# Optimization experiments

Measured on AMD Instinct MI355X. Metric: run time of the kernel, lower is better.

The kernel has to match this reference:

```python
import jax, jax.numpy as jnp
import numpy as np

N_NODES = 100000
N_EDGES = 1600000
N_GRAPHS = 512


def setup_inputs() -> dict:
    key = jax.random.key(0)
    k = jax.random.split(key, 6)
    x = jax.random.normal(k[0], (N_NODES, 768), dtype=jnp.float32)
    edge_index = jax.random.randint(k[1], (2, N_EDGES), 0, N_NODES, dtype=jnp.int32)
    batch = jnp.sort(jax.random.randint(k[2], (N_NODES,), 0, N_GRAPHS, dtype=jnp.int32))
    W1 = jax.random.normal(k[3], (768, 256), dtype=jnp.float32) * 0.02
    b1 = jnp.zeros((256,), dtype=jnp.float32)
    W2 = jax.random.normal(k[4], (256, 2), dtype=jnp.float32) * 0.02
    b2 = jnp.zeros((2,), dtype=jnp.float32)
    return {"x": x, "edge_index": edge_index, "batch": batch,
            "W1": W1, "b1": b1, "W2": W2, "b2": b2}


def gcn_conv(x, src, dst, W, b, n_nodes):
    # PyG GCNConv: h = x @ W; add self-loops; symmetric normalization D^-1/2 A D^-1/2
    h = x @ W  # [N, out]
    ones = jnp.ones((src.shape[0],), dtype=x.dtype)
    # degree including self-loop
    deg = jax.ops.segment_sum(ones, dst, num_segments=n_nodes) + 1.0  # [N]
    dinv = jax.lax.rsqrt(deg)
    norm_e = dinv[src] * dinv[dst]  # [E]
    msg = h[src] * norm_e[:, None]  # gather + scale, [E, out]
    agg = jax.ops.segment_sum(msg, dst, num_segments=n_nodes)  # scatter-add
    # self-loop contribution: norm = dinv[i]*dinv[i] = 1/deg[i]
    agg = agg + h * (1.0 / deg)[:, None]
    return agg + b


def reference(x, edge_index, batch, W1, b1, W2, b2):
    n_nodes = x.shape[0]
    src, dst = edge_index[0], edge_index[1]
    h = gcn_conv(x, src, dst, W1, b1, n_nodes)
    h = jax.nn.relu(h)
    # dropout p=0.5 is identity in eval mode (self.training=False)
    h = gcn_conv(h, src, dst, W2, b2, n_nodes)
    # global_mean_pool over batch assignment
    sums = jax.ops.segment_sum(h, batch, num_segments=N_GRAPHS)  # [G, out]
    counts = jax.ops.segment_sum(jnp.ones((n_nodes,), h.dtype), batch, num_segments=N_GRAPHS)
    return sums / jnp.maximum(counts, 1.0)[:, None]
```

## Files before the change

### kernel.cpp

```cpp
#include <hip/hip_runtime.h>

typedef unsigned short u16;
typedef unsigned int   u32;
typedef __bf16 bf16x8 __attribute__((ext_vector_type(8)));
typedef float  f32x4  __attribute__((ext_vector_type(4)));
typedef u32    u32x4  __attribute__((ext_vector_type(4)));
typedef u16    u16x8  __attribute__((ext_vector_type(8)));

#define NF1 768
#define NF2 256

__device__ __forceinline__ u16 f2bf(float f) {
  u32 u = __builtin_bit_cast(u32, f);
  u += 0x7fffu + ((u >> 16) & 1u);
  return (u16)(u >> 16);
}
__device__ __forceinline__ float bf2f(u16 h) {
  return __builtin_bit_cast(float, ((u32)h) << 16);
}

__device__ __forceinline__ void gll16(const void* g, void* l) {
  __builtin_amdgcn_global_load_lds(
      (const __attribute__((address_space(1))) unsigned int*)g,
      (__attribute__((address_space(3))) unsigned int*)l, 16, 0, 0);
}

__global__ void k_zero(u32* __restrict__ p, int n) {
  int i = blockIdx.x * 256 + threadIdx.x;
  if (i < n) p[i] = 0u;
}

__global__ void k_w1t(const float* __restrict__ W1, u16* __restrict__ W1T) {
  int idx = blockIdx.x * 256 + threadIdx.x;
  if (idx < NF1 * NF2) {
    int k = idx >> 8, j = idx & 255;
    W1T[(size_t)j * NF1 + k] = f2bf(W1[idx]);
  }
}

__global__ __launch_bounds__(512, 1) void k_gemm(const float* __restrict__ X,
                                                 const u16* __restrict__ W1T,
                                                 u16* __restrict__ H1, int M) {
  __shared__ float lsA[256 * 64];
  __shared__ u16   lsB[256 * 64];
  const int t    = threadIdx.x;
  const int m0   = blockIdx.x * 256;
  const int lane = t & 63;
  const int wid  = t >> 6;
  const int wr   = wid >> 1;
  const int wc   = wid & 1;

  const float* srcA[8];
  #pragma unroll
  for (int i = 0; i < 8; ++i) {
    int row_l = wid * 32 + i * 4 + (lane >> 4);
    int perm  = ((row_l & 7) << 1) | ((row_l >> 3) & 1);
    int gr    = m0 + row_l;
    if (gr > M - 1) gr = M - 1;
    srcA[i] = X + (size_t)gr * NF1 + (((lane & 15) ^ perm) * 4);
  }
  const u16* srcB[4];
  #pragma unroll
  for (int j = 0; j < 4; ++j) {
    int col_l = wid * 32 + j * 8 + (lane >> 3);
    srcB[j] = W1T + (size_t)col_l * NF1 + (((lane & 7) ^ (lane >> 3)) * 8);
  }

  f32x4 acc[4][8];
  #pragma unroll
  for (int m = 0; m < 4; ++m)
    #pragma unroll
    for (int n = 0; n < 8; ++n) { f32x4 z = {0.f, 0.f, 0.f, 0.f}; acc[m][n] = z; }

  const int lm     = lane & 15;
  const int l4     = lane >> 4;
  const int perm_r = ((lane & 7) << 1) | ((lane >> 3) & 1);
  const int lp     = lane & 7;

  const int NT = NF1 / 64;
  for (int kt = 0; kt < NT; ++kt) {
    #pragma unroll
    for (int i = 0; i < 8; ++i)
      gll16(srcA[i] + kt * 64, &lsA[(wid * 32 + i * 4) * 64]);
    #pragma unroll
    for (int j = 0; j < 4; ++j)
      gll16(srcB[j] + kt * 64, &lsB[(wid * 32 + j * 8) * 64]);
    __syncthreads();

    #pragma unroll
    for (int ks = 0; ks < 2; ++ks) {
      bf16x8 af[4], bfr[8];
      const int c = ks * 4 + l4;
      #pragma unroll
      for (int m = 0; m < 4; ++m) {
        int row = wr * 64 + m * 16 + lm;
        int ulo = (2 * c) ^ perm_r;
        const char* base = (const char*)lsA + row * 256;
        float4 L = *(const float4*)(base + ulo * 16);
        float4 H = *(const float4*)(base + (ulo ^ 1) * 16);
        u32 w0, w1, w2, w3;
        asm("v_cvt_pk_bf16_f32 %0, %1, %2" : "=v"(w0) : "v"(L.x), "v"(L.y));
        asm("v_cvt_pk_bf16_f32 %0, %1, %2" : "=v"(w1) : "v"(L.z), "v"(L.w));
        asm("v_cvt_pk_bf16_f32 %0, %1, %2" : "=v"(w2) : "v"(H.x), "v"(H.y));
        asm("v_cvt_pk_bf16_f32 %0, %1, %2" : "=v"(w3) : "v"(H.z), "v"(H.w));
        u32x4 uw = {w0, w1, w2, w3};
        af[m] = __builtin_bit_cast(bf16x8, uw);
      }
      #pragma unroll
      for (int n = 0; n < 8; ++n) {
        int col = wc * 128 + n * 16 + lm;
        int ph  = c ^ lp;
        bfr[n] = *(const bf16x8*)((const char*)lsB + col * 128 + ph * 16);
      }
      #pragma unroll
      for (int m = 0; m < 4; ++m)
        #pragma unroll
        for (int n = 0; n < 8; ++n)
          acc[m][n] = __builtin_amdgcn_mfma_f32_16x16x32_bf16(af[m], bfr[n], acc[m][n], 0, 0, 0);
    }
    __syncthreads();
  }

  #pragma unroll
  for (int m = 0; m < 4; ++m) {
    int rowb = m0 + wr * 64 + m * 16 + (lane >> 4) * 4;
    #pragma unroll
    for (int n = 0; n < 8; ++n) {
      int col = wc * 128 + n * 16 + (lane & 15);
      #pragma unroll
      for (int j = 0; j < 4; ++j) {
        int row = rowb + j;
        if (row < M) H1[(size_t)row * NF2 + col] = f2bf(acc[m][n][j]);
      }
    }
  }
}

__global__ void k_deg(const int* __restrict__ EI, int E, u32* __restrict__ deg) {
  int e = blockIdx.x * 256 + threadIdx.x;
  if (e < E) atomicAdd(&deg[EI[E + e]], 1u);
}

__global__ __launch_bounds__(1024) void k_scan1(const u32* __restrict__ deg,
                                                u32* __restrict__ rowptr,
                                                u32* __restrict__ bsum, int Nn) {
  __shared__ u32 sm[1024];
  int t = threadIdx.x;
  int i = blockIdx.x * 1024 + t;
  u32 v = (i < Nn) ? deg[i] : 0u;
  sm[t] = v;
  __syncthreads();
  #pragma unroll
  for (int off = 1; off < 1024; off <<= 1) {
    u32 x = (t >= off) ? sm[t - off] : 0u;
    __syncthreads();
    sm[t] += x;
    __syncthreads();
  }
  u32 incl = sm[t];
  if (i < Nn) rowptr[i] = incl - v;
  if (t == 1023) bsum[blockIdx.x] = incl;
}

__global__ void k_scan2(const u32* __restrict__ bsum, u32* __restrict__ boff, int nc) {
  __shared__ u32 sm[128];
  int t = threadIdx.x;
  u32 v = (t < nc) ? bsum[t] : 0u;
  sm[t] = v;
  __syncthreads();
  #pragma unroll
  for (int off = 1; off < 128; off <<= 1) {
    u32 x = (t >= off) ? sm[t - off] : 0u;
    __syncthreads();
    sm[t] += x;
    __syncthreads();
  }
  if (t < nc) boff[t] = sm[t] - v;
}

__global__ void k_scan3(u32* __restrict__ rowptr, const u32* __restrict__ boff,
                        u32* __restrict__ cursor, const u32* __restrict__ deg,
                        float* __restrict__ dinv, int Nn, int E) {
  int i = blockIdx.x * 256 + threadIdx.x;
  if (i < Nn) {
    u32 rp = rowptr[i] + boff[i >> 10];
    rowptr[i] = rp;
    cursor[i] = rp;
    dinv[i] = rsqrtf((float)deg[i] + 1.0f);
  }
  if (i == 0) rowptr[Nn] = (u32)E;
}

__global__ void k_fill(const int* __restrict__ EI, int E, int* __restrict__ cursor,
                       int* __restrict__ csr) {
  int e = blockIdx.x * 256 + threadIdx.x;
  if (e < E) {
    int s = EI[e], d = EI[E + e];
    int pos = atomicAdd(&cursor[d], 1);
    csr[pos] = s;
  }
}

__global__ __launch_bounds__(256) void k_agg1(const u16* __restrict__ H1,
                                              const int* __restrict__ csr,
                                              const u32* __restrict__ rowptr,
                                              const float* __restrict__ dinv,
                                              const float* __restrict__ B1,
                                              const float* __restrict__ W2,
                                              float* __restrict__ H2, int Nn) {
  int node = (blockIdx.x << 2) + (threadIdx.x >> 6);
  if (node >= Nn) return;
  const int lane = threadIdx.x & 63;
  const int hl   = lane >> 5;
  const int fo   = (lane & 31) * 8;
  const int rp0 = (int)rowptr[node], rp1 = (int)rowptr[node + 1];
  const float dvi = dinv[node];

  float c0 = 0.f, c1 = 0.f, c2 = 0.f, c3 = 0.f,
        c4 = 0.f, c5 = 0.f, c6 = 0.f, c7 = 0.f;

  for (int e = rp0 + 2 * hl; e < rp1; e += 8) {
    const int eA = e, eB = e + 1, eC = e + 4, eD = e + 5;
    const bool hB = eB < rp1, hC = eC < rp1, hD = eD < rp1;
    const int sA = csr[eA];
    const int sB = hB ? csr[eB] : sA;
    const int sC = hC ? csr[eC] : sA;
    const int sD = hD ? csr[eD] : sA;
    const u16x8 rA = *(const u16x8*)(H1 + (size_t)sA * NF2 + fo);
    const u16x8 rB = *(const u16x8*)(H1 + (size_t)sB * NF2 + fo);
    const u16x8 rC = *(const u16x8*)(H1 + (size_t)sC * NF2 + fo);
    const u16x8 rD = *(const u16x8*)(H1 + (size_t)sD * NF2 + fo);
    const float nA = dinv[sA] * dvi;
    const float nB = hB ? dinv[sB] * dvi : 0.f;
    const float nC = hC ? dinv[sC] * dvi : 0.f;
    const float nD = hD ? dinv[sD] * dvi : 0.f;
    c0 += nA * bf2f(rA[0]) + nB * bf2f(rB[0]) + nC * bf2f(rC[0]) + nD * bf2f(rD[0]);
    c1 += nA * bf2f(rA[1]) + nB * bf2f(rB[1]) + nC * bf2f(rC[1]) + nD * bf2f(rD[1]);
    c2 += nA * bf2f(rA[2]) + nB * bf2f(rB[2]) + nC * bf2f(rC[2]) + nD * bf2f(rD[2]);
    c3 += nA * bf2f(rA[3]) + nB * bf2f(rB[3]) + nC * bf2f(rC[3]) + nD * bf2f(rD[3]);
    c4 += nA * bf2f(rA[4]) + nB * bf2f(rB[4]) + nC * bf2f(rC[4]) + nD * bf2f(rD[4]);
    c5 += nA * bf2f(rA[5]) + nB * bf2f(rB[5]) + nC * bf2f(rC[5]) + nD * bf2f(rD[5]);
    c6 += nA * bf2f(rA[6]) + nB * bf2f(rB[6]) + nC * bf2f(rC[6]) + nD * bf2f(rD[6]);
    c7 += nA * bf2f(rA[7]) + nB * bf2f(rB[7]) + nC * bf2f(rC[7]) + nD * bf2f(rD[7]);
  }

  c0 += __shfl_xor(c0, 32);
  c1 += __shfl_xor(c1, 32);
  c2 += __shfl_xor(c2, 32);
  c3 += __shfl_xor(c3, 32);
  c4 += __shfl_xor(c4, 32);
  c5 += __shfl_xor(c5, 32);
  c6 += __shfl_xor(c6, 32);
  c7 += __shfl_xor(c7, 32);

  {
    const float ns = dvi * dvi;
    const u16x8 rs = *(const u16x8*)(H1 + (size_t)node * NF2 + fo);
    c0 += ns * bf2f(rs[0]); c1 += ns * bf2f(rs[1]);
    c2 += ns * bf2f(rs[2]); c3 += ns * bf2f(rs[3]);
    c4 += ns * bf2f(rs[4]); c5 += ns * bf2f(rs[5]);
    c6 += ns * bf2f(rs[6]); c7 += ns * bf2f(rs[7]);
  }

  const float4 bA = *(const float4*)(B1 + fo);
  const float4 bB = *(const float4*)(B1 + fo + 4);
  const float r0 = fmaxf(c0 + bA.x, 0.f), r1 = fmaxf(c1 + bA.y, 0.f);
  const float r2 = fmaxf(c2 + bA.z, 0.f), r3 = fmaxf(c3 + bA.w, 0.f);
  const float r4 = fmaxf(c4 + bB.x, 0.f), r5 = fmaxf(c5 + bB.y, 0.f);
  const float r6 = fmaxf(c6 + bB.z, 0.f), r7 = fmaxf(c7 + bB.w, 0.f);

  const float4* wp = (const float4*)(W2 + 2 * fo);
  const float4 w0 = wp[0], w1 = wp[1], w2 = wp[2], w3 = wp[3];
  float p0 = r0 * w0.x + r1 * w0.z + r2 * w1.x + r3 * w1.z
           + r4 * w2.x + r5 * w2.z + r6 * w3.x + r7 * w3.z;
  float p1 = r0 * w0.y + r1 * w0.w + r2 * w1.y + r3 * w1.w
           + r4 * w2.y + r5 * w2.w + r6 * w3.y + r7 * w3.w;
  #pragma unroll
  for (int o = 16; o; o >>= 1) {
    p0 += __shfl_xor(p0, o);
    p1 += __shfl_xor(p1, o);
  }
  if (lane == 0) {
    H2[2 * (size_t)node]     = p0;
    H2[2 * (size_t)node + 1] = p1;
  }
}

__global__ __launch_bounds__(256) void k_l2e(const int* __restrict__ EI, int E,
                                             const float* __restrict__ dinv,
                                             const float* __restrict__ H2,
                                             const int* __restrict__ batch,
                                             float* __restrict__ accg) {
  __shared__ float sb[1024];
  for (int i = threadIdx.x; i < 1024; i += 256) sb[i] = 0.f;
  __syncthreads();
  for (int e = blockIdx.x * 256 + threadIdx.x; e < E; e += gridDim.x * 256) {
    int s = EI[e], d = EI[E + e];
    float nrm = dinv[s] * dinv[d];
    float2 hv = *(const float2*)(H2 + 2 * (size_t)s);
    int g = batch[d];
    atomicAdd(&sb[2 * g],     nrm * hv.x);
    atomicAdd(&sb[2 * g + 1], nrm * hv.y);
  }
  __syncthreads();
  for (int i = threadIdx.x; i < 1024; i += 256)
    if (sb[i] != 0.f) atomicAdd(&accg[i], sb[i]);
}

__global__ __launch_bounds__(256) void k_l2n(int Nn, const float* __restrict__ dinv,
                                             const float* __restrict__ H2,
                                             const int* __restrict__ batch,
                                             float* __restrict__ accg,
                                             u32* __restrict__ gcnt) {
  __shared__ float sb[1024];
  __shared__ u32 sc[512];
  for (int i = threadIdx.x; i < 1024; i += 256) sb[i] = 0.f;
  for (int i = threadIdx.x; i < 512; i += 256) sc[i] = 0u;
  __syncthreads();
  for (int i = blockIdx.x * 256 + threadIdx.x; i < Nn; i += gridDim.x * 256) {
    int g = batch[i];
    float dv = dinv[i];
    float ns = dv * dv;
    float2 hv = *(const float2*)(H2 + 2 * (size_t)i);
    atomicAdd(&sb[2 * g],     ns * hv.x);
    atomicAdd(&sb[2 * g + 1], ns * hv.y);
    atomicAdd(&sc[g], 1u);
  }
  __syncthreads();
  for (int i = threadIdx.x; i < 1024; i += 256)
    if (sb[i] != 0.f) atomicAdd(&accg[i], sb[i]);
  for (int i = threadIdx.x; i < 512; i += 256)
    if (sc[i]) atomicAdd(&gcnt[i], sc[i]);
}

__global__ void k_final(const float* __restrict__ accg, const u32* __restrict__ gcnt,
                        const float* __restrict__ B2, float* __restrict__ out) {
  int i = blockIdx.x * 256 + threadIdx.x;
  if (i < 1024) {
    int g = i >> 1, c = i & 1;
    float cnt = (float)gcnt[g];
    float s = accg[i] + cnt * B2[c];
    out[i] = s / fmaxf(cnt, 1.0f);
  }
}

extern "C" void kernel_launch(void* const* d_in, const int* in_sizes, int n_in,
                              void* d_out, int out_size, void* d_ws, size_t ws_size,
                              hipStream_t stream) {
  const float* X     = (const float*)d_in[0];
  const int*   EI    = (const int*)d_in[1];
  const int*   BATCH = (const int*)d_in[2];
  const float* W1    = (const float*)d_in[3];
  const float* B1    = (const float*)d_in[4];
  const float* W2    = (const float*)d_in[5];
  const float* B2    = (const float*)d_in[6];
  const int Nn = in_sizes[0] / NF1;
  const int E  = in_sizes[1] / 2;
  float* OUT = (float*)d_out;
  (void)n_in; (void)out_size; (void)ws_size;

  char* w = (char*)d_ws;
  size_t off = 0;
  auto alloc = [&](size_t bytes) -> void* {
    void* p = w + off;
    off = (off + bytes + 511) & ~(size_t)511;
    return p;
  };
  u32*   deg    = (u32*)alloc((size_t)Nn * 4);
  u32*   rowptr = (u32*)alloc(((size_t)Nn + 1) * 4);
  u32*   cursor = (u32*)alloc((size_t)Nn * 4);
  u32*   bsum   = (u32*)alloc(512);
  u32*   boff   = (u32*)alloc(512);
  float* dinv   = (float*)alloc((size_t)Nn * 4);
  int*   csr    = (int*)alloc((size_t)E * 4);
  u16*   H1     = (u16*)alloc((size_t)Nn * NF2 * 2);
  float* H2     = (float*)alloc((size_t)Nn * 2 * 4);
  float* accg   = (float*)alloc(1536 * 4);
  u32*   gcnt   = (u32*)(accg + 1024);
  u16*   W1T    = (u16*)alloc((size_t)NF1 * NF2 * 2);

  const int NC = (Nn + 1023) >> 10;

  hipLaunchKernelGGL(k_zero, dim3((Nn + 255) / 256), dim3(256), 0, stream, deg, Nn);
  hipLaunchKernelGGL(k_zero, dim3(6), dim3(256), 0, stream, (u32*)accg, 1536);
  hipLaunchKernelGGL(k_w1t, dim3((NF1 * NF2 + 255) / 256), dim3(256), 0, stream, W1, W1T);
  hipLaunchKernelGGL(k_gemm, dim3((Nn + 255) / 256), dim3(512), 0, stream, X, W1T, H1, Nn);
  hipLaunchKernelGGL(k_deg, dim3((E + 255) / 256), dim3(256), 0, stream, EI, E, deg);
  hipLaunchKernelGGL(k_scan1, dim3(NC), dim3(1024), 0, stream, deg, rowptr, bsum, Nn);
  hipLaunchKernelGGL(k_scan2, dim3(1), dim3(128), 0, stream, bsum, boff, NC);
  hipLaunchKernelGGL(k_scan3, dim3((Nn + 255) / 256), dim3(256), 0, stream,
                     rowptr, boff, cursor, deg, dinv, Nn, E);
  hipLaunchKernelGGL(k_fill, dim3((E + 255) / 256), dim3(256), 0, stream,
                     EI, E, (int*)cursor, csr);
  hipLaunchKernelGGL(k_agg1, dim3((Nn + 3) / 4), dim3(256), 0, stream,
                     H1, csr, rowptr, dinv, B1, W2, H2, Nn);
  hipLaunchKernelGGL(k_l2e, dim3(512), dim3(256), 0, stream, EI, E, dinv, H2, BATCH, accg);
  hipLaunchKernelGGL(k_l2n, dim3(256), dim3(256), 0, stream, Nn, dinv, H2, BATCH, accg, gcnt);
  hipLaunchKernelGGL(k_final, dim3(4), dim3(256), 0, stream, accg, gcnt, B2, OUT);
}
```

Baseline: 474.8 us.

## Prescale GEMM rows by dinv, widen gather unroll, fuse layer-2 pooling kernels

The GEMM epilogue now multiplies each row by dinv[row], so the aggregation kernel no longer loads dinv per neighbour. It just sums pre-scaled rows and applies the destination dinv once at the end. Out-of-range edges are redirected to a zero padding row, and the loop is unrolled to 8 edges per iteration for more memory parallelism. The two layer-2 pooling kernels are merged into one that reads dinv and graph id packed together in PB, and G2 is stored pre-scaled by dinv. Rounding to bf16 after scaling changes numerics slightly, and the GEMM now has to wait for the degree scan.

```diff
diff --git a/kernel.cpp b/kernel.cpp
--- a/kernel.cpp
+++ b/kernel.cpp
@@ -40,7 +40,8 @@
 
 __global__ __launch_bounds__(512, 1) void k_gemm(const float* __restrict__ X,
                                                  const u16* __restrict__ W1T,
-                                                 u16* __restrict__ H1, int M) {
+                                                 const float* __restrict__ dinv,
+                                                 u16* __restrict__ H1s, int M) {
   __shared__ float lsA[256 * 64];
   __shared__ u16   lsB[256 * 64];
   const int t    = threadIdx.x;
@@ -125,12 +126,15 @@
   for (int m = 0; m < 4; ++m) {
     int rowb = m0 + wr * 64 + m * 16 + (lane >> 4) * 4;
     #pragma unroll
-    for (int n = 0; n < 8; ++n) {
-      int col = wc * 128 + n * 16 + (lane & 15);
-      #pragma unroll
-      for (int j = 0; j < 4; ++j) {
-        int row = rowb + j;
-        if (row < M) H1[(size_t)row * NF2 + col] = f2bf(acc[m][n][j]);
+    for (int j = 0; j < 4; ++j) {
+      int row = rowb + j;
+      if (row < M) {
+        float dv = dinv[row];
+        #pragma unroll
+        for (int n = 0; n < 8; ++n) {
+          int col = wc * 128 + n * 16 + (lane & 15);
+          H1s[(size_t)row * NF2 + col] = f2bf(dv * acc[m][n][j]);
+        }
       }
     }
   }
@@ -180,13 +184,17 @@
 
 __global__ void k_scan3(u32* __restrict__ rowptr, const u32* __restrict__ boff,
                         u32* __restrict__ cursor, const u32* __restrict__ deg,
-                        float* __restrict__ dinv, int Nn, int E) {
+                        float* __restrict__ dinv, const int* __restrict__ batch,
+                        float* __restrict__ PB, int Nn, int E) {
   int i = blockIdx.x * 256 + threadIdx.x;
   if (i < Nn) {
     u32 rp = rowptr[i] + boff[i >> 10];
     rowptr[i] = rp;
     cursor[i] = rp;
-    dinv[i] = rsqrtf((float)deg[i] + 1.0f);
+    float dv = rsqrtf((float)deg[i] + 1.0f);
+    dinv[i] = dv;
+    PB[2 * i]     = dv;
+    PB[2 * i + 1] = __builtin_bit_cast(float, batch[i]);
   }
   if (i == 0) rowptr[Nn] = (u32)E;
 }
@@ -201,13 +209,13 @@
   }
 }
 
-__global__ __launch_bounds__(256) void k_agg1(const u16* __restrict__ H1,
+__global__ __launch_bounds__(256) void k_agg1(const u16* __restrict__ H1s,
                                               const int* __restrict__ csr,
                                               const u32* __restrict__ rowptr,
                                               const float* __restrict__ dinv,
                                               const float* __restrict__ B1,
                                               const float* __restrict__ W2,
-                                              float* __restrict__ H2, int Nn) {
+                                              float* __restrict__ G2, int Nn) {
   int node = (blockIdx.x << 2) + (threadIdx.x >> 6);
   if (node >= Nn) return;
   const int lane = threadIdx.x & 63;
@@ -219,29 +227,41 @@
   float c0 = 0.f, c1 = 0.f, c2 = 0.f, c3 = 0.f,
         c4 = 0.f, c5 = 0.f, c6 = 0.f, c7 = 0.f;
 
-  for (int e = rp0 + 2 * hl; e < rp1; e += 8) {
-    const int eA = e, eB = e + 1, eC = e + 4, eD = e + 5;
-    const bool hB = eB < rp1, hC = eC < rp1, hD = eD < rp1;
+  for (int e = rp0 + 2 * hl; e < rp1; e += 16) {
+    const int eA = e,      eB = e + 1,  eC = e + 4,  eD = e + 5;
+    const int eE = e + 8,  eF = e + 9,  eG = e + 12, eH = e + 13;
     const int sA = csr[eA];
-    const int sB = hB ? csr[eB] : sA;
-    const int sC = hC ? csr[eC] : sA;
-    const int sD = hD ? csr[eD] : sA;
-    const u16x8 rA = *(const u16x8*)(H1 + (size_t)sA * NF2 + fo);
-    const u16x8 rB = *(const u16x8*)(H1 + (size_t)sB * NF2 + fo);
-    const u16x8 rC = *(const u16x8*)(H1 + (size_t)sC * NF2 + fo);
-    const u16x8 rD = *(const u16x8*)(H1 + (size_t)sD * NF2 + fo);
-    const float nA = dinv[sA] * dvi;
-    const float nB = hB ? dinv[sB] * dvi : 0.f;
-    const float nC = hC ? dinv[sC] * dvi : 0.f;
-    const float nD = hD ? dinv[sD] * dvi : 0.f;
-    c0 += nA * bf2f(rA[0]) + nB * bf2f(rB[0]) + nC * bf2f(rC[0]) + nD * bf2f(rD[0]);
-    c1 += nA * bf2f(rA[1]) + nB * bf2f(rB[1]) + nC * bf2f(rC[1]) + nD * bf2f(rD[1]);
-    c2 += nA * bf2f(rA[2]) + nB * bf2f(rB[2]) + nC * bf2f(rC[2]) + nD * bf2f(rD[2]);
-    c3 += nA * bf2f(rA[3]) + nB * bf2f(rB[3]) + nC * bf2f(rC[3]) + nD * bf2f(rD[3]);
-    c4 += nA * bf2f(rA[4]) + nB * bf2f(rB[4]) + nC * bf2f(rC[4]) + nD * bf2f(rD[4]);
-    c5 += nA * bf2f(rA[5]) + nB * bf2f(rB[5]) + nC * bf2f(rC[5]) + nD * bf2f(rD[5]);
-    c6 += nA * bf2f(rA[6]) + nB * bf2f(rB[6]) + nC * bf2f(rC[6]) + nD * bf2f(rD[6]);
-    c7 += nA * bf2f(rA[7]) + nB * bf2f(rB[7]) + nC * bf2f(rC[7]) + nD * bf2f(rD[7]);
+    const int sB = (eB < rp1) ? csr[eB] : Nn;
+    const int sC = (eC < rp1) ? csr[eC] : Nn;
+    const int sD = (eD < rp1) ? csr[eD] : Nn;
+    const int sE = (eE < rp1) ? csr[eE] : Nn;
+    const int sF = (eF < rp1) ? csr[eF] : Nn;
+    const int sG = (eG < rp1) ? csr[eG] : Nn;
+    const int sH = (eH < rp1) ? csr[eH] : Nn;
+    const u16x8 rA = *(const u16x8*)(H1s + (size_t)sA * NF2 + fo);
+    const u16x8 rB = *(const u16x8*)(H1s + (size_t)sB * NF2 + fo);
+    const u16x8 rC = *(const u16x8*)(H1s + (size_t)sC * NF2 + fo);
+    const u16x8 rD = *(const u16x8*)(H1s + (size_t)sD * NF2 + fo);
+    const u16x8 rE = *(const u16x8*)(H1s + (size_t)sE * NF2 + fo);
+    const u16x8 rF = *(const u16x8*)(H1s + (size_t)sF * NF2 + fo);
+    const u16x8 rG = *(const u16x8*)(H1s + (size_t)sG * NF2 + fo);
+    const u16x8 rH = *(const u16x8*)(H1s + (size_t)sH * NF2 + fo);
+    c0 += bf2f(rA[0]) + bf2f(rB[0]) + bf2f(rC[0]) + bf2f(rD[0])
+        + bf2f(rE[0]) + bf2f(rF[0]) + bf2f(rG[0]) + bf2f(rH[0]);
+    c1 += bf2f(rA[1]) + bf2f(rB[1]) + bf2f(rC[1]) + bf2f(rD[1])
+        + bf2f(rE[1]) + bf2f(rF[1]) + bf2f(rG[1]) + bf2f(rH[1]);
+    c2 += bf2f(rA[2]) + bf2f(rB[2]) + bf2f(rC[2]) + bf2f(rD[2])
+        + bf2f(rE[2]) + bf2f(rF[2]) + bf2f(rG[2]) + bf2f(rH[2]);
+    c3 += bf2f(rA[3]) + bf2f(rB[3]) + bf2f(rC[3]) + bf2f(rD[3])
+        + bf2f(rE[3]) + bf2f(rF[3]) + bf2f(rG[3]) + bf2f(rH[3]);
+    c4 += bf2f(rA[4]) + bf2f(rB[4]) + bf2f(rC[4]) + bf2f(rD[4])
+        + bf2f(rE[4]) + bf2f(rF[4]) + bf2f(rG[4]) + bf2f(rH[4]);
+    c5 += bf2f(rA[5]) + bf2f(rB[5]) + bf2f(rC[5]) + bf2f(rD[5])
+        + bf2f(rE[5]) + bf2f(rF[5]) + bf2f(rG[5]) + bf2f(rH[5]);
+    c6 += bf2f(rA[6]) + bf2f(rB[6]) + bf2f(rC[6]) + bf2f(rD[6])
+        + bf2f(rE[6]) + bf2f(rF[6]) + bf2f(rG[6]) + bf2f(rH[6]);
+    c7 += bf2f(rA[7]) + bf2f(rB[7]) + bf2f(rC[7]) + bf2f(rD[7])
+        + bf2f(rE[7]) + bf2f(rF[7]) + bf2f(rG[7]) + bf2f(rH[7]);
   }
 
   c0 += __shfl_xor(c0, 32);
@@ -254,20 +274,19 @@
   c7 += __shfl_xor(c7, 32);
 
   {
-    const float ns = dvi * dvi;
-    const u16x8 rs = *(const u16x8*)(H1 + (size_t)node * NF2 + fo);
-    c0 += ns * bf2f(rs[0]); c1 += ns * bf2f(rs[1]);
-    c2 += ns * bf2f(rs[2]); c3 += ns * bf2f(rs[3]);
-    c4 += ns * bf2f(rs[4]); c5 += ns * bf2f(rs[5]);
-    c6 += ns * bf2f(rs[6]); c7 += ns * bf2f(rs[7]);
+    const u16x8 rs = *(const u16x8*)(H1s + (size_t)node * NF2 + fo);
+    c0 += bf2f(rs[0]); c1 += bf2f(rs[1]);
+    c2 += bf2f(rs[2]); c3 += bf2f(rs[3]);
+    c4 += bf2f(rs[4]); c5 += bf2f(rs[5]);
+    c6 += bf2f(rs[6]); c7 += bf2f(rs[7]);
   }
 
   const float4 bA = *(const float4*)(B1 + fo);
   const float4 bB = *(const float4*)(B1 + fo + 4);
-  const float r0 = fmaxf(c0 + bA.x, 0.f), r1 = fmaxf(c1 + bA.y, 0.f);
-  const float r2 = fmaxf(c2 + bA.z, 0.f), r3 = fmaxf(c3 + bA.w, 0.f);
-  const float r4 = fmaxf(c4 + bB.x, 0.f), r5 = fmaxf(c5 + bB.y, 0.f);
-  const float r6 = fmaxf(c6 + bB.z, 0.f), r7 = fmaxf(c7 + bB.w, 0.f);
+  const float r0 = fmaxf(dvi * c0 + bA.x, 0.f), r1 = fmaxf(dvi * c1 + bA.y, 0.f);
+  const float r2 = fmaxf(dvi * c2 + bA.z, 0.f), r3 = fmaxf(dvi * c3 + bA.w, 0.f);
+  const float r4 = fmaxf(dvi * c4 + bB.x, 0.f), r5 = fmaxf(dvi * c5 + bB.y, 0.f);
+  const float r6 = fmaxf(dvi * c6 + bB.z, 0.f), r7 = fmaxf(dvi * c7 + bB.w, 0.f);
 
   const float4* wp = (const float4*)(W2 + 2 * fo);
   const float4 w0 = wp[0], w1 = wp[1], w2 = wp[2], w3 = wp[3];
@@ -281,49 +300,36 @@
     p1 += __shfl_xor(p1, o);
   }
   if (lane == 0) {
-    H2[2 * (size_t)node]     = p0;
-    H2[2 * (size_t)node + 1] = p1;
-  }
-}
-
-__global__ __launch_bounds__(256) void k_l2e(const int* __restrict__ EI, int E,
-                                             const float* __restrict__ dinv,
-                                             const float* __restrict__ H2,
-                                             const int* __restrict__ batch,
-                                             float* __restrict__ accg) {
-  __shared__ float sb[1024];
-  for (int i = threadIdx.x; i < 1024; i += 256) sb[i] = 0.f;
-  __syncthreads();
-  for (int e = blockIdx.x * 256 + threadIdx.x; e < E; e += gridDim.x * 256) {
-    int s = EI[e], d = EI[E + e];
-    float nrm = dinv[s] * dinv[d];
-    float2 hv = *(const float2*)(H2 + 2 * (size_t)s);
-    int g = batch[d];
-    atomicAdd(&sb[2 * g],     nrm * hv.x);
-    atomicAdd(&sb[2 * g + 1], nrm * hv.y);
-  }
-  __syncthreads();
-  for (int i = threadIdx.x; i < 1024; i += 256)
-    if (sb[i] != 0.f) atomicAdd(&accg[i], sb[i]);
-}
-
-__global__ __launch_bounds__(256) void k_l2n(int Nn, const float* __restrict__ dinv,
-                                             const float* __restrict__ H2,
-                                             const int* __restrict__ batch,
-                                             float* __restrict__ accg,
-                                             u32* __restrict__ gcnt) {
+    G2[2 * (size_t)node]     = dvi * p0;
+    G2[2 * (size_t)node + 1] = dvi * p1;
+  }
+}
+
+__global__ __launch_bounds__(256) void k_l2(const int* __restrict__ EI, int E,
+                                            const float* __restrict__ PB,
+                                            const float* __restrict__ G2,
+                                            int Nn,
+                                            float* __restrict__ accg,
+                                            u32* __restrict__ gcnt) {
   __shared__ float sb[1024];
   __shared__ u32 sc[512];
   for (int i = threadIdx.x; i < 1024; i += 256) sb[i] = 0.f;
   for (int i = threadIdx.x; i < 512; i += 256) sc[i] = 0u;
   __syncthreads();
+  for (int e = blockIdx.x * 256 + threadIdx.x; e < E; e += gridDim.x * 256) {
+    int s = EI[e], d = EI[E + e];
+    float2 pb = *(const float2*)(PB + 2 * (size_t)d);
+    float2 hv = *(const float2*)(G2 + 2 * (size_t)s);
+    int g = __builtin_bit_cast(int, pb.y);
+    atomicAdd(&sb[2 * g],     pb.x * hv.x);
+    atomicAdd(&sb[2 * g + 1], pb.x * hv.y);
+  }
   for (int i = blockIdx.x * 256 + threadIdx.x; i < Nn; i += gridDim.x * 256) {
-    int g = batch[i];
-    float dv = dinv[i];
-    float ns = dv * dv;
-    float2 hv = *(const float2*)(H2 + 2 * (size_t)i);
-    atomicAdd(&sb[2 * g],     ns * hv.x);
-    atomicAdd(&sb[2 * g + 1], ns * hv.y);
+    float2 pb = *(const float2*)(PB + 2 * (size_t)i);
+    float2 hv = *(const float2*)(G2 + 2 * (size_t)i);
+    int g = __builtin_bit_cast(int, pb.y);
+    atomicAdd(&sb[2 * g],     pb.x * hv.x);
+    atomicAdd(&sb[2 * g + 1], pb.x * hv.y);
     atomicAdd(&sc[g], 1u);
   }
   __syncthreads();
@@ -372,9 +378,10 @@
   u32*   bsum   = (u32*)alloc(512);
   u32*   boff   = (u32*)alloc(512);
   float* dinv   = (float*)alloc((size_t)Nn * 4);
+  float* PB     = (float*)alloc((size_t)Nn * 8);
   int*   csr    = (int*)alloc((size_t)E * 4);
-  u16*   H1     = (u16*)alloc((size_t)Nn * NF2 * 2);
-  float* H2     = (float*)alloc((size_t)Nn * 2 * 4);
+  u16*   H1s    = (u16*)alloc(((size_t)Nn + 1) * NF2 * 2);
+  float* G2     = (float*)alloc((size_t)Nn * 2 * 4);
   float* accg   = (float*)alloc(1536 * 4);
   u32*   gcnt   = (u32*)(accg + 1024);
   u16*   W1T    = (u16*)alloc((size_t)NF1 * NF2 * 2);
@@ -383,18 +390,20 @@
 
   hipLaunchKernelGGL(k_zero, dim3((Nn + 255) / 256), dim3(256), 0, stream, deg, Nn);
   hipLaunchKernelGGL(k_zero, dim3(6), dim3(256), 0, stream, (u32*)accg, 1536);
-  hipLaunchKernelGGL(k_w1t, dim3((NF1 * NF2 + 255) / 256), dim3(256), 0, stream, W1, W1T);
-  hipLaunchKernelGGL(k_gemm, dim3((Nn + 255) / 256), dim3(512), 0, stream, X, W1T, H1, Nn);
+  hipLaunchKernelGGL(k_zero, dim3(1), dim3(256), 0, stream,
+                     (u32*)(H1s + (size_t)Nn * NF2), NF2 / 2);
   hipLaunchKernelGGL(k_deg, dim3((E + 255) / 256), dim3(256), 0, stream, EI, E, deg);
   hipLaunchKernelGGL(k_scan1, dim3(NC), dim3(1024), 0, stream, deg, rowptr, bsum, Nn);
   hipLaunchKernelGGL(k_scan2, dim3(1), dim3(128), 0, stream, bsum, boff, NC);
   hipLaunchKernelGGL(k_scan3, dim3((Nn + 255) / 256), dim3(256), 0, stream,
-                     rowptr, boff, cursor, deg, dinv, Nn, E);
+                     rowptr, boff, cursor, deg, dinv, BATCH, PB, Nn, E);
+  hipLaunchKernelGGL(k_w1t, dim3((NF1 * NF2 + 255) / 256), dim3(256), 0, stream, W1, W1T);
+  hipLaunchKernelGGL(k_gemm, dim3((Nn + 255) / 256), dim3(512), 0, stream,
+                     X, W1T, dinv, H1s, Nn);
   hipLaunchKernelGGL(k_fill, dim3((E + 255) / 256), dim3(256), 0, stream,
                      EI, E, (int*)cursor, csr);
   hipLaunchKernelGGL(k_agg1, dim3((Nn + 3) / 4), dim3(256), 0, stream,
-                     H1, csr, rowptr, dinv, B1, W2, H2, Nn);
-  hipLaunchKernelGGL(k_l2e, dim3(512), dim3(256), 0, stream, EI, E, dinv, H2, BATCH, accg);
-  hipLaunchKernelGGL(k_l2n, dim3(256), dim3(256), 0, stream, Nn, dinv, H2, BATCH, accg, gcnt);
+                     H1s, csr, rowptr, dinv, B1, W2, G2, Nn);
+  hipLaunchKernelGGL(k_l2, dim3(256), dim3(256), 0, stream, EI, E, PB, G2, Nn, accg, gcnt);
   hipLaunchKernelGGL(k_final, dim3(4), dim3(256), 0, stream, accg, gcnt, B2, OUT);
 }
```

New measurement: 421.1 us. -11.3%, faster.
